# Kernel optimization log

Hardware: AMD Instinct MI355X
Metric: run time of the kernel (lower is better)

## Reference

```python
import jax, jax.numpy as jnp
import numpy as np

B, S, H = 1, 4096, 2048
NH, NKV = 16, 4
HD = H // NH  # 128
GROUPS = NH // NKV


def setup_inputs() -> dict:
    key = jax.random.key(0)
    ks = jax.random.split(key, 5)
    hidden_states = jax.random.normal(ks[0], (B, S, H), dtype=jnp.float32)
    # causal additive mask: 0 on/below diagonal, large negative above
    neg = jnp.finfo(jnp.float32).min
    causal = jnp.where(jnp.tril(jnp.ones((S, S), dtype=bool)), 0.0, neg)
    attention_mask = jnp.broadcast_to(causal, (B, 1, S, S)).astype(jnp.float32)
    sc = 0.02
    Wq = jax.random.normal(ks[1], (H, NH * HD), dtype=jnp.float32) * sc
    Wk = jax.random.normal(ks[2], (H, NKV * HD), dtype=jnp.float32) * sc
    Wv = jax.random.normal(ks[3], (H, NKV * HD), dtype=jnp.float32) * sc
    Wo = jax.random.normal(ks[4], (H, H), dtype=jnp.float32) * sc
    return {"hidden_states": hidden_states, "attention_mask": attention_mask,
            "Wq": Wq, "Wk": Wk, "Wv": Wv, "Wo": Wo}


def reference(hidden_states, attention_mask, Wq, Wk, Wv, Wo):
    b, s, _ = hidden_states.shape
    # projections -> (b, heads, s, hd)
    q = (hidden_states @ Wq).reshape(b, s, NH, HD).transpose(0, 2, 1, 3)
    k = (hidden_states @ Wk).reshape(b, s, NKV, HD).transpose(0, 2, 1, 3)
    v = (hidden_states @ Wv).reshape(b, s, NKV, HD).transpose(0, 2, 1, 3)
    # repeat_kv for GQA: (b, nkv, s, hd) -> (b, nh, s, hd)
    k = jnp.repeat(k, GROUPS, axis=1)
    v = jnp.repeat(v, GROUPS, axis=1)
    scores = jnp.einsum('bhqd,bhkd->bhqk', q, k) / jnp.sqrt(jnp.float32(HD))
    scores = scores + attention_mask
    attn = jax.nn.softmax(scores.astype(jnp.float32), axis=-1).astype(q.dtype)
    out = jnp.einsum('bhqk,bhkd->bhqd', attn, v)
    out = out.transpose(0, 2, 1, 3).reshape(b, s, H)
    return out @ Wo
```

## Files before the change

kernel.cpp:

```cpp
#include <hip/hip_runtime.h>


typedef __bf16 bf16;
typedef float f32x4 __attribute__((ext_vector_type(4)));
typedef float f32x16 __attribute__((ext_vector_type(16)));
typedef bf16 bf16x4 __attribute__((ext_vector_type(4)));
typedef bf16 bf16x8 __attribute__((ext_vector_type(8)));
typedef unsigned u32x4 __attribute__((ext_vector_type(4)));

#define MFMA16(A, B, C) __builtin_amdgcn_mfma_f32_16x16x32_bf16((A), (B), (C), 0, 0, 0)
#define MFMA32(A, B, C) __builtin_amdgcn_mfma_f32_32x32x16_bf16((A), (B), (C), 0, 0, 0)

__device__ __forceinline__ void async16(const bf16* g, bf16* l) {
  __builtin_amdgcn_global_load_lds(
      (const __attribute__((address_space(1))) unsigned int*)g,
      (__attribute__((address_space(3))) unsigned int*)l, 16, 0, 0);
}

__device__ __forceinline__ float exp2v(float x) {
  float r; asm("v_exp_f32 %0, %1" : "=v"(r) : "v"(x)); return r;
}
__device__ __forceinline__ unsigned cvtpk(float a, float b) {
  unsigned r; asm("v_cvt_pk_bf16_f32 %0, %1, %2" : "=v"(r) : "v"(a), "v"(b)); return r;
}
#define PLSWAP(a, b) asm("v_permlane32_swap_b32 %0, %1" : "+v"(a), "+v"(b))

__device__ __forceinline__ bf16x8 mkfrag(unsigned a0, unsigned a1,
                                         unsigned c0, unsigned c1) {
  PLSWAP(a0, c0);
  PLSWAP(a1, c1);
  u32x4 t = {a0, a1, c0, c1};
  return __builtin_bit_cast(bf16x8, t);
}

__global__ void cast_bf16_kernel(const float* __restrict__ in,
                                 bf16* __restrict__ out, int n4) {
  int i = blockIdx.x * blockDim.x + threadIdx.x;
  int stride = gridDim.x * blockDim.x;
  for (; i < n4; i += stride) {
    float4 v = ((const float4*)in)[i];
    bf16x4 o = {(bf16)v.x, (bf16)v.y, (bf16)v.z, (bf16)v.w};
    ((bf16x4*)out)[i] = o;
  }
}

__global__ void transpose_cast_kernel(const float* __restrict__ src, int srcCols,
                                      bf16* __restrict__ dst, float scale) {
  __shared__ float t[64][65];
  const int kt = blockIdx.y * 64;
  const int nt = blockIdx.x * 64;
  const int r0 = threadIdx.x >> 4;
  const int c0 = (threadIdx.x & 15) * 4;
#pragma unroll
  for (int i = 0; i < 4; ++i) {
    int r = r0 + i * 16;
    float4 v = *(const float4*)(src + (kt + r) * srcCols + nt + c0);
    t[r][c0 + 0] = v.x; t[r][c0 + 1] = v.y; t[r][c0 + 2] = v.z; t[r][c0 + 3] = v.w;
  }
  __syncthreads();
#pragma unroll
  for (int i = 0; i < 4; ++i) {
    int r = r0 + i * 16;
    bf16x4 b = {(bf16)(t[c0 + 0][r] * scale), (bf16)(t[c0 + 1][r] * scale),
                (bf16)(t[c0 + 2][r] * scale), (bf16)(t[c0 + 3][r] * scale)};
    *(bf16x4*)(dst + (nt + r) * 2048 + kt + c0) = b;
  }
}

template <int MODE>
__global__ __launch_bounds__(256, 2) void gemm_bt(
    const bf16* __restrict__ A, const bf16* __restrict__ BT, int K,
    bf16* __restrict__ Qb, bf16* __restrict__ Kb, bf16* __restrict__ Vt,
    float* __restrict__ Cf) {
  __shared__ bf16 As[128 * 32];
  __shared__ bf16 Bs[128 * 32];
  const int tid = threadIdx.x;
  const int w = tid >> 6, lane = tid & 63, g = lane >> 4, lq = lane & 15;
  const int wr = w >> 1, wc = w & 1;
  const int mBase = blockIdx.y * 128, nBase = blockIdx.x * 128;

  f32x4 acc[4][4] = {};
  const int KT = K >> 5;
  for (int kt = 0; kt < KT; ++kt) {
#pragma unroll
    for (int r = 0; r < 2; ++r) {
      int chunk = r * 256 + tid;
      int row = chunk >> 2, cu = chunk & 3;
      async16(A + (mBase + row) * K + kt * 32 + cu * 8, As + (r * 256 + w * 64) * 8);
      async16(BT + (nBase + row) * K + kt * 32 + cu * 8, Bs + (r * 256 + w * 64) * 8);
    }
    asm volatile("s_waitcnt vmcnt(0)" ::: "memory");
    __syncthreads();

    bf16x8 af[4], bfr[4];
#pragma unroll
    for (int i = 0; i < 4; ++i)
      af[i] = *(const bf16x8*)(As + (wr * 64 + i * 16 + lq) * 32 + g * 8);
#pragma unroll
    for (int i = 0; i < 4; ++i)
      bfr[i] = *(const bf16x8*)(Bs + (wc * 64 + i * 16 + lq) * 32 + g * 8);
#pragma unroll
    for (int mi = 0; mi < 4; ++mi)
#pragma unroll
      for (int ni = 0; ni < 4; ++ni)
        acc[mi][ni] = MFMA16(af[mi], bfr[ni], acc[mi][ni]);
    __syncthreads();
  }

#pragma unroll
  for (int mi = 0; mi < 4; ++mi)
#pragma unroll
    for (int ni = 0; ni < 4; ++ni) {
      const int n = nBase + wc * 64 + ni * 16 + lq;
      const int m0 = mBase + wr * 64 + mi * 16 + 4 * g;
      if (MODE == 0) {
        if (nBase < 2048) {
#pragma unroll
          for (int jr = 0; jr < 4; ++jr)
            Qb[(m0 + jr) * 2048 + n] = (bf16)acc[mi][ni][jr];
        } else if (nBase < 2560) {
#pragma unroll
          for (int jr = 0; jr < 4; ++jr)
            Kb[(m0 + jr) * 512 + (n - 2048)] = (bf16)acc[mi][ni][jr];
        } else {
          bf16x4 v = {(bf16)acc[mi][ni][0], (bf16)acc[mi][ni][1],
                      (bf16)acc[mi][ni][2], (bf16)acc[mi][ni][3]};
          *(bf16x4*)(Vt + (n - 2560) * 4096 + m0) = v;
        }
      } else {
#pragma unroll
        for (int jr = 0; jr < 4; ++jr)
          Cf[(m0 + jr) * 2048 + n] = acc[mi][ni][jr];
      }
    }
}

__global__ __launch_bounds__(256, 2) void attn_fwd(
    const bf16* __restrict__ Qb,
    const bf16* __restrict__ Kb,
    const bf16* __restrict__ Vt,
    bf16* __restrict__ AO) {
  __shared__ __align__(16) bf16 Ks[2][64 * 128];
  __shared__ __align__(16) bf16 Vs[128 * 64];

  const int bid = blockIdx.x;
  const int h = bid & 15;
  const int qt = (bid < 256) ? (bid >> 4) : (31 - ((bid - 256) >> 4));
  const int kv = h >> 2;
  const int tid = threadIdx.x;
  const int w = tid >> 6, lane = tid & 63, l5 = lane & 31, g2 = lane >> 5;
  const int sxr = (l5 & 7) << 4;
  const int qbase = qt * 128;
  const int nk = 2 * (qt + 1);
  const int qw = qbase + w * 32 + l5;

  bf16x8 aq[8];
  {
    const bf16* qrow = Qb + qw * 2048 + h * 128;
#pragma unroll
    for (int kk = 0; kk < 8; ++kk)
      aq[kk] = *(const bf16x8*)(qrow + kk * 16 + g2 * 8);
  }

  float mst = -1e30f, lst = 0.f;
  f32x16 o[4] = {};

  auto STAGE_K = [&](int t, int buf) {
#pragma unroll
    for (int r = 0; r < 4; ++r) {
      int gid = r * 256 + tid;
      int krow = gid >> 4, cu = gid & 15;
      async16(Kb + (t * 64 + krow) * 512 + kv * 128 + ((cu ^ (krow & 7)) * 8),
              &Ks[buf][(r * 256 + w * 64) * 8]);
    }
  };
  auto STAGE_V = [&](int t) {
#pragma unroll
    for (int r = 0; r < 4; ++r) {
      int gid = r * 256 + tid;
      int vrow = gid >> 3, gv = gid & 7;
      async16(Vt + (kv * 128 + vrow) * 4096 + t * 64 + ((gv ^ (vrow & 7)) * 8),
              &Vs[(r * 256 + w * 64) * 8]);
    }
  };

  STAGE_K(0, 0);
  STAGE_V(0);
  STAGE_K(1, 1);
  asm volatile("s_waitcnt vmcnt(8)" ::: "memory");
  __builtin_amdgcn_s_barrier();
  __builtin_amdgcn_sched_barrier(0);

  f32x16 s0 = {}, s1 = {};
  {
    const char* kb0 = (const char*)&Ks[0][0] + l5 * 256;
    __builtin_amdgcn_s_setprio(1);
#pragma unroll
    for (int kk = 0; kk < 8; ++kk) {
      const int off = (kk * 32 + g2 * 16) ^ sxr;
      bf16x8 k0 = *(const bf16x8*)(kb0 + off);
      bf16x8 k1 = *(const bf16x8*)(kb0 + 8192 + off);
      s0 = MFMA32(k0, aq[kk], s0);
      s1 = MFMA32(k1, aq[kk], s1);
    }
    __builtin_amdgcn_s_setprio(0);
  }
  __builtin_amdgcn_sched_barrier(0);
  __builtin_amdgcn_s_barrier();

  for (int t = 0; t < nk; ++t) {
    const int cur = t & 1, nxt = (t + 1) & 1;

    STAGE_K(min(t + 2, nk - 1), cur);

    if (t >= 2 * qt) {
      const int kb = t * 64 + 4 * g2;
#pragma unroll
      for (int r = 0; r < 16; ++r) {
        const int key = kb + (r & 3) + 8 * (r >> 2);
        if (key > qw) s0[r] = -1e30f;
        if (key + 32 > qw) s1[r] = -1e30f;
      }
    }

    {
      float mx[16];
#pragma unroll
      for (int r = 0; r < 16; ++r) mx[r] = fmaxf(s0[r], s1[r]);
#pragma unroll
      for (int off = 8; off > 0; off >>= 1)
#pragma unroll
        for (int r = 0; r < off; ++r) mx[r] = fmaxf(mx[r], mx[r + off]);
      const float pm = fmaxf(mx[0], __shfl_xor(mx[0], 32));

      if (__any(pm > mst + 8.f)) {
        const float mn = fmaxf(mst, pm);
        const float al = exp2v(mst - mn);
        mst = mn;
        lst *= al;
#pragma unroll
        for (int dt = 0; dt < 4; ++dt)
#pragma unroll
          for (int r = 0; r < 16; ++r) o[dt][r] *= al;
      }
#pragma unroll
      for (int r = 0; r < 16; ++r) {
        s0[r] = exp2v(s0[r] - mst);
        s1[r] = exp2v(s1[r] - mst);
      }
      float sm[16];
#pragma unroll
      for (int r = 0; r < 16; ++r) sm[r] = s0[r] + s1[r];
#pragma unroll
      for (int off = 8; off > 0; off >>= 1)
#pragma unroll
        for (int r = 0; r < off; ++r) sm[r] += sm[r + off];
      lst += sm[0] + __shfl_xor(sm[0], 32);
    }

    bf16x8 pb[4];
    {
      unsigned pw0[8], pw1[8];
#pragma unroll
      for (int wi = 0; wi < 8; ++wi) {
        pw0[wi] = cvtpk(s0[2 * wi], s0[2 * wi + 1]);
        pw1[wi] = cvtpk(s1[2 * wi], s1[2 * wi + 1]);
      }
      pb[0] = mkfrag(pw0[0], pw0[1], pw0[2], pw0[3]);
      pb[1] = mkfrag(pw0[4], pw0[5], pw0[6], pw0[7]);
      pb[2] = mkfrag(pw1[0], pw1[1], pw1[2], pw1[3]);
      pb[3] = mkfrag(pw1[4], pw1[5], pw1[6], pw1[7]);
    }

    asm volatile("s_waitcnt vmcnt(4)" ::: "memory");
    __builtin_amdgcn_s_barrier();
    __builtin_amdgcn_sched_barrier(0);

    f32x16 n0 = {}, n1 = {};
    const char* kb0 = (const char*)&Ks[nxt][0] + l5 * 256;
    const char* vb0 = (const char*)&Vs[0];
    if (t + 1 < nk) {
      __builtin_amdgcn_s_setprio(1);
#pragma unroll
      for (int i = 0; i < 8; ++i) {
        const int koff = (i * 32 + g2 * 16) ^ sxr;
        bf16x8 k0 = *(const bf16x8*)(kb0 + koff);
        bf16x8 k1 = *(const bf16x8*)(kb0 + 8192 + koff);
        n0 = MFMA32(k0, aq[i], n0);
        n1 = MFMA32(k1, aq[i], n1);
        {
          const int j = 2 * i, dt = j & 3, KK = j >> 2;
          bf16x8 av = *(const bf16x8*)(vb0 + (dt * 32 + l5) * 128 +
                                       ((KK * 32 + g2 * 16) ^ sxr));
          o[dt] = MFMA32(av, pb[KK], o[dt]);
        }
        {
          const int j = 2 * i + 1, dt = j & 3, KK = j >> 2;
          bf16x8 av = *(const bf16x8*)(vb0 + (dt * 32 + l5) * 128 +
                                       ((KK * 32 + g2 * 16) ^ sxr));
          o[dt] = MFMA32(av, pb[KK], o[dt]);
        }
      }
      __builtin_amdgcn_s_setprio(0);
    } else {
      __builtin_amdgcn_s_setprio(1);
#pragma unroll
      for (int j = 0; j < 16; ++j) {
        const int dt = j & 3, KK = j >> 2;
        bf16x8 av = *(const bf16x8*)(vb0 + (dt * 32 + l5) * 128 +
                                     ((KK * 32 + g2 * 16) ^ sxr));
        o[dt] = MFMA32(av, pb[KK], o[dt]);
      }
      __builtin_amdgcn_s_setprio(0);
    }
    __builtin_amdgcn_sched_barrier(0);
    __builtin_amdgcn_s_barrier();

    if (t + 1 < nk) STAGE_V(t + 1);

    s0 = n0;
    s1 = n1;
  }

  {
    const float inv = 1.f / lst;
    bf16* aob = AO + qw * 2048 + h * 128;
#pragma unroll
    for (int dt = 0; dt < 4; ++dt)
#pragma unroll
      for (int m = 0; m < 4; ++m) {
        bf16x4 ov = {(bf16)(o[dt][4 * m + 0] * inv), (bf16)(o[dt][4 * m + 1] * inv),
                     (bf16)(o[dt][4 * m + 2] * inv), (bf16)(o[dt][4 * m + 3] * inv)};
        *(bf16x4*)(aob + dt * 32 + 8 * m + 4 * g2) = ov;
      }
  }
}

extern "C" void kernel_launch(void* const* d_in, const int* in_sizes, int n_in,
                              void* d_out, int out_size, void* d_ws, size_t ws_size,
                              hipStream_t stream) {
  const float* X = (const float*)d_in[0];
  const float* Wq = (const float*)d_in[2];
  const float* Wk = (const float*)d_in[3];
  const float* Wv = (const float*)d_in[4];
  const float* Wo = (const float*)d_in[5];
  float* out = (float*)d_out;
  char* ws = (char*)d_ws;

  bf16* Xb = (bf16*)ws;
  bf16* WT = (bf16*)(ws + 16777216);
  bf16* Qb = (bf16*)(ws + 29360128);
  bf16* Kb = (bf16*)(ws + 46137344);
  bf16* Vt = (bf16*)(ws + 50331648);

  cast_bf16_kernel<<<2048, 256, 0, stream>>>(X, Xb, (4096 * 2048) / 4);
  transpose_cast_kernel<<<dim3(32, 32), 256, 0, stream>>>(
      Wq, 2048, WT, 0.08838834764831845f * 1.4426950408889634f);
  transpose_cast_kernel<<<dim3(8, 32), 256, 0, stream>>>(Wk, 512, WT + 2048 * 2048, 1.0f);
  transpose_cast_kernel<<<dim3(8, 32), 256, 0, stream>>>(Wv, 512, WT + 2560 * 2048, 1.0f);

  gemm_bt<0><<<dim3(24, 32), 256, 0, stream>>>(Xb, WT, 2048, Qb, Kb, Vt, (float*)nullptr);

  transpose_cast_kernel<<<dim3(32, 32), 256, 0, stream>>>(Wo, 2048, WT, 1.0f);

  attn_fwd<<<512, 256, 0, stream>>>(Qb, Kb, Vt, Xb);

  gemm_bt<1><<<dim3(16, 32), 256, 0, stream>>>(Xb, WT, 2048, (bf16*)nullptr,
                                               (bf16*)nullptr, (bf16*)nullptr, out);
}
```

Before: 253.8 us.

## Compute softmax row sums via MFMA with ones, use max3, fuse QKV weight transposes

Replaces the per-tile softmax denominator reduction (adds plus a cross-lane shuffle) with an extra MFMA that multiplies a ones fragment by the probability fragments, accumulating row sums on the matrix unit. The max reduction is rewritten with v_max3 instructions to cut VALU ops. The three separate Q/K/V weight transpose-cast launches are merged into one kernel launch. These trade VALU work for extra MFMA issue slots and an extra 16-register accumulator, which may raise register pressure in the attention kernel.

```diff
diff --git a/kernel.cpp b/kernel.cpp
--- a/kernel.cpp
+++ b/kernel.cpp
@@ -22,6 +22,9 @@
 }
 __device__ __forceinline__ unsigned cvtpk(float a, float b) {
   unsigned r; asm("v_cvt_pk_bf16_f32 %0, %1, %2" : "=v"(r) : "v"(a), "v"(b)); return r;
+}
+__device__ __forceinline__ float max3f(float a, float b, float c) {
+  float r; asm("v_max3_f32 %0, %1, %2, %3" : "=v"(r) : "v"(a), "v"(b), "v"(c)); return r;
 }
 #define PLSWAP(a, b) asm("v_permlane32_swap_b32 %0, %1" : "+v"(a), "+v"(b))
 
@@ -64,6 +67,43 @@
     bf16x4 b = {(bf16)(t[c0 + 0][r] * scale), (bf16)(t[c0 + 1][r] * scale),
                 (bf16)(t[c0 + 2][r] * scale), (bf16)(t[c0 + 3][r] * scale)};
     *(bf16x4*)(dst + (nt + r) * 2048 + kt + c0) = b;
+  }
+}
+
+__global__ void transpose_qkv_kernel(const float* __restrict__ Wq,
+                                     const float* __restrict__ Wk,
+                                     const float* __restrict__ Wv,
+                                     bf16* __restrict__ WT) {
+  __shared__ float t[64][65];
+  const int bx = blockIdx.x;
+  const float* src;
+  int srcCols, ntl, dstRow;
+  float scale;
+  if (bx < 32) {
+    src = Wq; srcCols = 2048; ntl = bx; dstRow = 0;
+    scale = 0.08838834764831845f * 1.4426950408889634f;
+  } else if (bx < 40) {
+    src = Wk; srcCols = 512; ntl = bx - 32; dstRow = 2048; scale = 1.0f;
+  } else {
+    src = Wv; srcCols = 512; ntl = bx - 40; dstRow = 2560; scale = 1.0f;
+  }
+  const int kt = blockIdx.y * 64;
+  const int nt = ntl * 64;
+  const int r0 = threadIdx.x >> 4;
+  const int c0 = (threadIdx.x & 15) * 4;
+#pragma unroll
+  for (int i = 0; i < 4; ++i) {
+    int r = r0 + i * 16;
+    float4 v = *(const float4*)(src + (kt + r) * srcCols + nt + c0);
+    t[r][c0 + 0] = v.x; t[r][c0 + 1] = v.y; t[r][c0 + 2] = v.z; t[r][c0 + 3] = v.w;
+  }
+  __syncthreads();
+#pragma unroll
+  for (int i = 0; i < 4; ++i) {
+    int r = r0 + i * 16;
+    bf16x4 b = {(bf16)(t[c0 + 0][r] * scale), (bf16)(t[c0 + 1][r] * scale),
+                (bf16)(t[c0 + 2][r] * scale), (bf16)(t[c0 + 3][r] * scale)};
+    *(bf16x4*)(WT + (dstRow + nt + r) * 2048 + kt + c0) = b;
   }
 }
 
@@ -154,6 +194,10 @@
   const int nk = 2 * (qt + 1);
   const int qw = qbase + w * 32 + l5;
 
+  const unsigned oo = 0x3F803F80u;
+  u32x4 ov4 = {oo, oo, oo, oo};
+  const bf16x8 ones = __builtin_bit_cast(bf16x8, ov4);
+
   bf16x8 aq[8];
   {
     const bf16* qrow = Qb + qw * 2048 + h * 128;
@@ -162,8 +206,9 @@
       aq[kk] = *(const bf16x8*)(qrow + kk * 16 + g2 * 8);
   }
 
-  float mst = -1e30f, lst = 0.f;
+  float mst = -1e30f;
   f32x16 o[4] = {};
+  f32x16 accl = {};
 
   auto STAGE_K = [&](int t, int buf) {
 #pragma unroll
@@ -227,17 +272,21 @@
       float mx[16];
 #pragma unroll
       for (int r = 0; r < 16; ++r) mx[r] = fmaxf(s0[r], s1[r]);
-#pragma unroll
-      for (int off = 8; off > 0; off >>= 1)
-#pragma unroll
-        for (int r = 0; r < off; ++r) mx[r] = fmaxf(mx[r], mx[r + off]);
-      const float pm = fmaxf(mx[0], __shfl_xor(mx[0], 32));
+      float a0 = max3f(mx[0], mx[1], mx[2]);
+      float a1 = max3f(mx[3], mx[4], mx[5]);
+      float a2 = max3f(mx[6], mx[7], mx[8]);
+      float a3 = max3f(mx[9], mx[10], mx[11]);
+      float a4 = max3f(mx[12], mx[13], mx[14]);
+      float b0 = max3f(a0, a1, a2);
+      float b1 = max3f(a3, a4, mx[15]);
+      const float lmax = fmaxf(b0, b1);
+      const float pm = fmaxf(lmax, __shfl_xor(lmax, 32));
 
       if (__any(pm > mst + 8.f)) {
         const float mn = fmaxf(mst, pm);
         const float al = exp2v(mst - mn);
         mst = mn;
-        lst *= al;
+        accl[0] *= al;
 #pragma unroll
         for (int dt = 0; dt < 4; ++dt)
 #pragma unroll
@@ -248,14 +297,6 @@
         s0[r] = exp2v(s0[r] - mst);
         s1[r] = exp2v(s1[r] - mst);
       }
-      float sm[16];
-#pragma unroll
-      for (int r = 0; r < 16; ++r) sm[r] = s0[r] + s1[r];
-#pragma unroll
-      for (int off = 8; off > 0; off >>= 1)
-#pragma unroll
-        for (int r = 0; r < off; ++r) sm[r] += sm[r + off];
-      lst += sm[0] + __shfl_xor(sm[0], 32);
     }
 
     bf16x8 pb[4];
@@ -300,6 +341,7 @@
                                        ((KK * 32 + g2 * 16) ^ sxr));
           o[dt] = MFMA32(av, pb[KK], o[dt]);
         }
+        if (i & 1) accl = MFMA32(ones, pb[i >> 1], accl);
       }
       __builtin_amdgcn_s_setprio(0);
     } else {
@@ -310,6 +352,7 @@
         bf16x8 av = *(const bf16x8*)(vb0 + (dt * 32 + l5) * 128 +
                                      ((KK * 32 + g2 * 16) ^ sxr));
         o[dt] = MFMA32(av, pb[KK], o[dt]);
+        if ((j & 3) == 3) accl = MFMA32(ones, pb[j >> 2], accl);
       }
       __builtin_amdgcn_s_setprio(0);
     }
@@ -323,7 +366,7 @@
   }
 
   {
-    const float inv = 1.f / lst;
+    const float inv = 1.f / accl[0];
     bf16* aob = AO + qw * 2048 + h * 128;
 #pragma unroll
     for (int dt = 0; dt < 4; ++dt)
@@ -354,10 +397,7 @@
   bf16* Vt = (bf16*)(ws + 50331648);
 
   cast_bf16_kernel<<<2048, 256, 0, stream>>>(X, Xb, (4096 * 2048) / 4);
-  transpose_cast_kernel<<<dim3(32, 32), 256, 0, stream>>>(
-      Wq, 2048, WT, 0.08838834764831845f * 1.4426950408889634f);
-  transpose_cast_kernel<<<dim3(8, 32), 256, 0, stream>>>(Wk, 512, WT + 2048 * 2048, 1.0f);
-  transpose_cast_kernel<<<dim3(8, 32), 256, 0, stream>>>(Wv, 512, WT + 2560 * 2048, 1.0f);
+  transpose_qkv_kernel<<<dim3(48, 32), 256, 0, stream>>>(Wq, Wk, Wv, WT);
 
   gemm_bt<0><<<dim3(24, 32), 256, 0, stream>>>(Xb, WT, 2048, Qb, Kb, Vt, (float*)nullptr);
 
```

New measurement: 340.2 us. 1.34x slower.
